# Performance work log

Measured on AMD Instinct MI355X. Metric: run time of the kernel, lower is better.

## Reference

```python
import jax, jax.numpy as jnp
import numpy as np

N = 16384   # src points
M = 16384   # ref points
D = 256     # d_embed
K = 16      # num_neighbors
MAX_DIST = 0.5


def _knn(src, ref, k):
    # squared euclidean distances, [N, M] (pytorch3d knn_points returns squared dists)
    d2 = (jnp.sum(src * src, axis=-1, keepdims=True)
          + jnp.sum(ref * ref, axis=-1)[None, :]
          - 2.0 * src @ ref.T)
    neg_d2, idx = jax.lax.top_k(-d2, k)   # k smallest distances, sorted ascending
    return -neg_d2, idx


def setup_inputs() -> dict:
    key = jax.random.key(0)
    k1, k2, k3, k4, k5 = jax.random.split(key, 5)
    return {
        "ref_points": jax.random.normal(k1, (M, 3), dtype=jnp.float32),
        "src_points": jax.random.normal(k2, (N, 3), dtype=jnp.float32),
        "ref_feats": jax.random.normal(k3, (M, D), dtype=jnp.float32),
        "src_feats": jax.random.normal(k4, (N, D), dtype=jnp.float32),
        "W": jax.random.normal(k5, (D, D), dtype=jnp.float32) * 0.1,
    }


def reference(ref_points, src_points, ref_feats, src_feats, W):
    dist, knn_idx = _knn(src_points, ref_points, K)      # [N,K], [N,K]
    knn_xyz = ref_points[knn_idx]                        # [N,K,3]
    weight = jax.nn.relu(1.0 - dist / MAX_DIST)          # [N,K]

    W_triu = jnp.triu(W)
    W_sym = W_triu + W_triu.T                            # symmetric bilinear form
    knn_feats = ref_feats[knn_idx]                       # [N,K,D]

    scores = jnp.einsum('nc,cd,nkd->nk', src_feats, W_sym, knn_feats)
    attn = jax.nn.softmax(scores * weight, axis=-1)      # [N,K]
    corres = jnp.einsum('nk,nkc->nc', attn, knn_xyz)     # [N,3]

    d = jnp.linalg.norm(src_points - corres, axis=-1)    # [N]
    w = jax.nn.relu(1.0 - d / MAX_DIST)                  # [N]
    return corres, w
```

## Files before the change

### kernel.cpp

```cpp
#include <hip/hip_runtime.h>
#include <math.h>

#define N_SRC 16384
#define M_REF 16384
#define DEMB  256
#define KNN_K 16
#define CAP   128

__global__ void wsym_kernel(const float* __restrict__ W, float* __restrict__ wsym) {
    int i = blockIdx.x;
    int j = threadIdx.x;
    float a = (j >= i) ? W[i * DEMB + j] : 0.f;
    float b = (i >= j) ? W[j * DEMB + i] : 0.f;
    wsym[i * DEMB + j] = a + b;
}

__global__ void pack_kernel(const float* __restrict__ rp, float4* __restrict__ out) {
    int i = blockIdx.x * 256 + threadIdx.x;
    float x = rp[i * 3 + 0], y = rp[i * 3 + 1], z = rp[i * 3 + 2];
    out[i] = make_float4(x, y, z, fmaf(x, x, fmaf(y, y, z * z)));
}

__global__ void __launch_bounds__(256) q_kernel(const float* __restrict__ src_feats,
                                                const float* __restrict__ wsym,
                                                float* __restrict__ q) {
    __shared__ __align__(16) float sf[32][DEMB];
    int n0 = blockIdx.x * 32;
    int tid = threadIdx.x;
    int c0 = tid & 63;
    int rg = tid >> 6;
    {
        int c = c0 * 4;
        #pragma unroll
        for (int rr = 0; rr < 8; ++rr) {
            int r = rr * 4 + rg;
            *(float4*)&sf[r][c] = *(const float4*)&src_feats[(size_t)(n0 + r) * DEMB + c];
        }
    }
    __syncthreads();

    float acc[8][4];
    #pragma unroll
    for (int rr = 0; rr < 8; ++rr)
        #pragma unroll
        for (int cc = 0; cc < 4; ++cc) acc[rr][cc] = 0.f;

    for (int c4 = 0; c4 < 64; ++c4) {
        float wv[4][4];
        #pragma unroll
        for (int j = 0; j < 4; ++j)
            #pragma unroll
            for (int cc = 0; cc < 4; ++cc)
                wv[j][cc] = wsym[(size_t)(c4 * 4 + j) * DEMB + c0 + cc * 64];
        #pragma unroll
        for (int rr = 0; rr < 8; ++rr) {
            float4 s = *(const float4*)&sf[rg * 8 + rr][c4 * 4];
            #pragma unroll
            for (int cc = 0; cc < 4; ++cc) {
                float a = acc[rr][cc];
                a = fmaf(s.x, wv[0][cc], a);
                a = fmaf(s.y, wv[1][cc], a);
                a = fmaf(s.z, wv[2][cc], a);
                a = fmaf(s.w, wv[3][cc], a);
                acc[rr][cc] = a;
            }
        }
    }
    #pragma unroll
    for (int rr = 0; rr < 8; ++rr)
        #pragma unroll
        for (int cc = 0; cc < 4; ++cc)
            q[(size_t)(n0 + rg * 8 + rr) * DEMB + (c0 + cc * 64)] = acc[rr][cc];
}

__device__ __forceinline__ void sort64_kv(float& vd, int& vi, int lane) {
    #pragma unroll
    for (int k = 2; k <= 64; k <<= 1) {
        #pragma unroll
        for (int j = k >> 1; j > 0; j >>= 1) {
            float od = __shfl_xor(vd, j, 64);
            int   oi = __shfl_xor(vi, j, 64);
            bool keep_min = (((lane & j) == 0) == ((lane & k) == 0));
            bool oless = (od < vd) || (od == vd && oi < vi);
            bool take = (keep_min == oless);
            vd = take ? od : vd;
            vi = take ? oi : vi;
        }
    }
}

__global__ void __launch_bounds__(128) knn_kernel(const float* __restrict__ src_points,
                                                  const float4* __restrict__ refp4,
                                                  float* __restrict__ kd2,
                                                  int* __restrict__ kidx) {
    const float INF = 3.0e38f;
    int tid = threadIdx.x;
    int h = tid >> 6, lane = tid & 63;
    int n0 = blockIdx.x * 8;

    __shared__ float cd[8][CAP];
    __shared__ int   ci[8][CAP];
    __shared__ int   cnt[8];
    if (tid < 8) cnt[tid] = 0;

    float m2x[8], m2y[8], m2z[8], sn2[8];
    #pragma unroll
    for (int b = 0; b < 8; ++b) {
        float sx = src_points[(n0 + b) * 3 + 0];
        float sy = src_points[(n0 + b) * 3 + 1];
        float sz = src_points[(n0 + b) * 3 + 2];
        m2x[b] = -2.f * sx; m2y[b] = -2.f * sy; m2z[b] = -2.f * sz;
        sn2[b] = fmaf(sx, sx, fmaf(sy, sy, sz * sz));
    }
    __syncthreads();

    const int base = h * (M_REF / 2);

    float mind[8];
    #pragma unroll
    for (int b = 0; b < 8; ++b) mind[b] = INF;
    for (int it = 0; it < 128; it += 2) {
        float4 r0 = refp4[base + it * 64 + lane];
        float4 r1 = refp4[base + (it + 1) * 64 + lane];
        #pragma unroll
        for (int b = 0; b < 8; ++b) {
            float d0 = fmaf(r0.x, m2x[b], r0.w);
            d0 = fmaf(r0.y, m2y[b], d0);
            d0 = fmaf(r0.z, m2z[b], d0);
            float d1 = fmaf(r1.x, m2x[b], r1.w);
            d1 = fmaf(r1.y, m2y[b], d1);
            d1 = fmaf(r1.z, m2z[b], d1);
            mind[b] = fminf(mind[b], fminf(d0, d1));
        }
    }

    float tau[8];
    #pragma unroll
    for (int b = 0; b < 8; ++b) {
        float v = mind[b];
        #pragma unroll
        for (int k = 2; k <= 64; k <<= 1) {
            #pragma unroll
            for (int j = k >> 1; j > 0; j >>= 1) {
                float o = __shfl_xor(v, j, 64);
                bool lower = (lane & j) == 0;
                bool up = (lane & k) == 0;
                float mn = fminf(v, o), mx = fmaxf(v, o);
                v = (lower == up) ? mn : mx;
            }
        }
        tau[b] = __shfl(v, 15, 64);
    }

    for (int it = 0; it < 128; it += 2) {
        int i0 = base + it * 64 + lane;
        float4 r0 = refp4[i0];
        float4 r1 = refp4[i0 + 64];
        #pragma unroll
        for (int b = 0; b < 8; ++b) {
            float d0 = fmaf(r0.x, m2x[b], r0.w);
            d0 = fmaf(r0.y, m2y[b], d0);
            d0 = fmaf(r0.z, m2z[b], d0);
            float d1 = fmaf(r1.x, m2x[b], r1.w);
            d1 = fmaf(r1.y, m2y[b], d1);
            d1 = fmaf(r1.z, m2z[b], d1);
            if (d0 <= tau[b]) {
                int p = atomicAdd(&cnt[b], 1);
                if (p < CAP) { cd[b][p] = d0; ci[b][p] = i0; }
            }
            if (d1 <= tau[b]) {
                int p = atomicAdd(&cnt[b], 1);
                if (p < CAP) { cd[b][p] = d1; ci[b][p] = i0 + 64; }
            }
        }
    }
    __syncthreads();

    #pragma unroll
    for (int bb = 0; bb < 4; ++bb) {
        int b = h * 4 + bb;
        int count = cnt[b];
        if (count > CAP) count = CAP;
        float vd = (lane < count) ? cd[b][lane] : INF;
        int   vi = (lane < count) ? ci[b][lane] : 0x7fffffff;
        sort64_kv(vd, vi, lane);
        int done = 64;
        while (done < count) {
            if (lane >= 16) {
                int p = done + (lane - 16);
                vd = (p < count) ? cd[b][p] : INF;
                vi = (p < count) ? ci[b][p] : 0x7fffffff;
            }
            sort64_kv(vd, vi, lane);
            done += 48;
        }
        if (lane < KNN_K) {
            kd2[(size_t)(n0 + b) * KNN_K + lane] = vd + sn2[b];
            kidx[(size_t)(n0 + b) * KNN_K + lane] = vi;
        }
    }
}

__global__ void __launch_bounds__(256) score_kernel(const float* __restrict__ q,
                                                    const float* __restrict__ ref_feats,
                                                    const float* __restrict__ ref_points,
                                                    const float* __restrict__ src_points,
                                                    const float* __restrict__ kd2,
                                                    const int* __restrict__ kidx,
                                                    float* __restrict__ out) {
    int wave = threadIdx.x >> 6;
    int lane = threadIdx.x & 63;
    int n = __builtin_amdgcn_readfirstlane(blockIdx.x * 4 + wave);

    float4 qv = *(const float4*)&q[(size_t)n * DEMB + lane * 4];

    int idx[KNN_K]; float d2[KNN_K];
    #pragma unroll
    for (int k = 0; k < KNN_K; ++k) {
        idx[k] = __builtin_amdgcn_readfirstlane(kidx[(size_t)n * KNN_K + k]);
        d2[k]  = kd2[(size_t)n * KNN_K + k];
    }

    float sc[KNN_K];
    #pragma unroll
    for (int k = 0; k < KNN_K; ++k) {
        float4 r = *(const float4*)&ref_feats[(size_t)idx[k] * DEMB + lane * 4];
        float p = fmaf(r.x, qv.x, fmaf(r.y, qv.y, fmaf(r.z, qv.z, r.w * qv.w)));
        #pragma unroll
        for (int off = 1; off < 64; off <<= 1) p += __shfl_xor(p, off, 64);
        sc[k] = p;
    }

    float tv[KNN_K];
    #pragma unroll
    for (int k = 0; k < KNN_K; ++k) {
        float wt = fmaxf(0.f, fmaf(-2.f, d2[k], 1.f));
        tv[k] = sc[k] * wt;
    }
    float m = tv[0];
    #pragma unroll
    for (int k = 1; k < KNN_K; ++k) m = fmaxf(m, tv[k]);
    float e[KNN_K], s = 0.f;
    #pragma unroll
    for (int k = 0; k < KNN_K; ++k) { e[k] = expf(tv[k] - m); s += e[k]; }

    float cx = 0.f, cy = 0.f, cz = 0.f;
    #pragma unroll
    for (int k = 0; k < KNN_K; ++k) {
        float rx = ref_points[idx[k] * 3 + 0];
        float ry = ref_points[idx[k] * 3 + 1];
        float rz = ref_points[idx[k] * 3 + 2];
        cx = fmaf(e[k], rx, cx);
        cy = fmaf(e[k], ry, cy);
        cz = fmaf(e[k], rz, cz);
    }
    float inv = 1.f / s;
    cx *= inv; cy *= inv; cz *= inv;

    if (lane == 0) {
        float ssx = src_points[n * 3 + 0];
        float ssy = src_points[n * 3 + 1];
        float ssz = src_points[n * 3 + 2];
        float dx = ssx - cx, dy = ssy - cy, dz = ssz - cz;
        float dist = sqrtf(fmaf(dx, dx, fmaf(dy, dy, dz * dz)));
        float w = fmaxf(0.f, fmaf(-2.f, dist, 1.f));
        out[(size_t)n * 3 + 0] = cx;
        out[(size_t)n * 3 + 1] = cy;
        out[(size_t)n * 3 + 2] = cz;
        out[(size_t)N_SRC * 3 + n] = w;
    }
}

extern "C" void kernel_launch(void* const* d_in, const int* in_sizes, int n_in,
                              void* d_out, int out_size, void* d_ws, size_t ws_size,
                              hipStream_t stream) {
    const float* ref_points = (const float*)d_in[0];
    const float* src_points = (const float*)d_in[1];
    const float* ref_feats  = (const float*)d_in[2];
    const float* src_feats  = (const float*)d_in[3];
    const float* W          = (const float*)d_in[4];
    float* out = (float*)d_out;

    float*  wsym  = (float*)d_ws;
    float4* refp4 = (float4*)(wsym + DEMB * DEMB);
    float*  q     = (float*)(refp4 + M_REF);
    float*  kd2   = q + (size_t)N_SRC * DEMB;
    int*    kidx  = (int*)(kd2 + (size_t)N_SRC * KNN_K);

    wsym_kernel<<<DEMB, DEMB, 0, stream>>>(W, wsym);
    pack_kernel<<<M_REF / 256, 256, 0, stream>>>(ref_points, refp4);
    q_kernel<<<N_SRC / 32, 256, 0, stream>>>(src_feats, wsym, q);
    knn_kernel<<<N_SRC / 8, 128, 0, stream>>>(src_points, refp4, kd2, kidx);
    score_kernel<<<N_SRC / 4, 256, 0, stream>>>(q, ref_feats, ref_points, src_points, kd2, kidx, out);
}
```

Before: 176.4 us.

## Fuse kNN and q-projection into one heterogeneous launch with 4-wave kNN blocks

After: 167.8 us. 1.05x faster.

```diff
diff --git a/kernel.cpp b/kernel.cpp
--- a/kernel.cpp
+++ b/kernel.cpp
@@ -5,7 +5,12 @@
 #define M_REF 16384
 #define DEMB  256
 #define KNN_K 16
-#define CAP   128
+#define CAP   288
+
+#define KNN_BLOCKS (N_SRC / 8)
+#define Q_BLOCKS   (N_SRC / 16)
+
+#define SMEM_BYTES (8 * CAP * 8 + 32 + 128)
 
 __global__ void wsym_kernel(const float* __restrict__ W, float* __restrict__ wsym) {
     int i = blockIdx.x;
@@ -19,58 +24,6 @@
     int i = blockIdx.x * 256 + threadIdx.x;
     float x = rp[i * 3 + 0], y = rp[i * 3 + 1], z = rp[i * 3 + 2];
     out[i] = make_float4(x, y, z, fmaf(x, x, fmaf(y, y, z * z)));
-}
-
-__global__ void __launch_bounds__(256) q_kernel(const float* __restrict__ src_feats,
-                                                const float* __restrict__ wsym,
-                                                float* __restrict__ q) {
-    __shared__ __align__(16) float sf[32][DEMB];
-    int n0 = blockIdx.x * 32;
-    int tid = threadIdx.x;
-    int c0 = tid & 63;
-    int rg = tid >> 6;
-    {
-        int c = c0 * 4;
-        #pragma unroll
-        for (int rr = 0; rr < 8; ++rr) {
-            int r = rr * 4 + rg;
-            *(float4*)&sf[r][c] = *(const float4*)&src_feats[(size_t)(n0 + r) * DEMB + c];
-        }
-    }
-    __syncthreads();
-
-    float acc[8][4];
-    #pragma unroll
-    for (int rr = 0; rr < 8; ++rr)
-        #pragma unroll
-        for (int cc = 0; cc < 4; ++cc) acc[rr][cc] = 0.f;
-
-    for (int c4 = 0; c4 < 64; ++c4) {
-        float wv[4][4];
-        #pragma unroll
-        for (int j = 0; j < 4; ++j)
-            #pragma unroll
-            for (int cc = 0; cc < 4; ++cc)
-                wv[j][cc] = wsym[(size_t)(c4 * 4 + j) * DEMB + c0 + cc * 64];
-        #pragma unroll
-        for (int rr = 0; rr < 8; ++rr) {
-            float4 s = *(const float4*)&sf[rg * 8 + rr][c4 * 4];
-            #pragma unroll
-            for (int cc = 0; cc < 4; ++cc) {
-                float a = acc[rr][cc];
-                a = fmaf(s.x, wv[0][cc], a);
-                a = fmaf(s.y, wv[1][cc], a);
-                a = fmaf(s.z, wv[2][cc], a);
-                a = fmaf(s.w, wv[3][cc], a);
-                acc[rr][cc] = a;
-            }
-        }
-    }
-    #pragma unroll
-    for (int rr = 0; rr < 8; ++rr)
-        #pragma unroll
-        for (int cc = 0; cc < 4; ++cc)
-            q[(size_t)(n0 + rg * 8 + rr) * DEMB + (c0 + cc * 64)] = acc[rr][cc];
 }
 
 __device__ __forceinline__ void sort64_kv(float& vd, int& vi, int lane) {
@@ -89,115 +42,176 @@
     }
 }
 
-__global__ void __launch_bounds__(128) knn_kernel(const float* __restrict__ src_points,
-                                                  const float4* __restrict__ refp4,
-                                                  float* __restrict__ kd2,
-                                                  int* __restrict__ kidx) {
-    const float INF = 3.0e38f;
+__global__ void __launch_bounds__(256, 8) fused_kernel(
+        const float* __restrict__ src_points, const float4* __restrict__ refp4,
+        const float* __restrict__ src_feats,  const float* __restrict__ wsym,
+        float* __restrict__ kd2, int* __restrict__ kidx, float* __restrict__ q) {
+    __shared__ __align__(16) char smem[SMEM_BYTES];
     int tid = threadIdx.x;
-    int h = tid >> 6, lane = tid & 63;
-    int n0 = blockIdx.x * 8;
-
-    __shared__ float cd[8][CAP];
-    __shared__ int   ci[8][CAP];
-    __shared__ int   cnt[8];
-    if (tid < 8) cnt[tid] = 0;
-
-    float m2x[8], m2y[8], m2z[8], sn2[8];
-    #pragma unroll
-    for (int b = 0; b < 8; ++b) {
-        float sx = src_points[(n0 + b) * 3 + 0];
-        float sy = src_points[(n0 + b) * 3 + 1];
-        float sz = src_points[(n0 + b) * 3 + 2];
-        m2x[b] = -2.f * sx; m2y[b] = -2.f * sy; m2z[b] = -2.f * sz;
-        sn2[b] = fmaf(sx, sx, fmaf(sy, sy, sz * sz));
-    }
-    __syncthreads();
-
-    const int base = h * (M_REF / 2);
-
-    float mind[8];
-    #pragma unroll
-    for (int b = 0; b < 8; ++b) mind[b] = INF;
-    for (int it = 0; it < 128; it += 2) {
-        float4 r0 = refp4[base + it * 64 + lane];
-        float4 r1 = refp4[base + (it + 1) * 64 + lane];
+
+    if (blockIdx.x < KNN_BLOCKS) {
+        const float INF = 3.0e38f;
+        float (*cd)[CAP] = (float(*)[CAP])smem;
+        int   (*ci)[CAP] = (int(*)[CAP])(smem + 8 * CAP * 4);
+        int*   cnt       = (int*)(smem + 8 * CAP * 8);
+        float (*stau)[8] = (float(*)[8])(smem + 8 * CAP * 8 + 32);
+
+        int h = tid >> 6, lane = tid & 63;
+        int n0 = blockIdx.x * 8;
+        if (tid < 8) cnt[tid] = 0;
+
+        float m2x[8], m2y[8], m2z[8], sn2[8];
         #pragma unroll
         for (int b = 0; b < 8; ++b) {
-            float d0 = fmaf(r0.x, m2x[b], r0.w);
-            d0 = fmaf(r0.y, m2y[b], d0);
-            d0 = fmaf(r0.z, m2z[b], d0);
-            float d1 = fmaf(r1.x, m2x[b], r1.w);
-            d1 = fmaf(r1.y, m2y[b], d1);
-            d1 = fmaf(r1.z, m2z[b], d1);
-            mind[b] = fminf(mind[b], fminf(d0, d1));
-        }
-    }
-
-    float tau[8];
-    #pragma unroll
-    for (int b = 0; b < 8; ++b) {
-        float v = mind[b];
-        #pragma unroll
-        for (int k = 2; k <= 64; k <<= 1) {
-            #pragma unroll
-            for (int j = k >> 1; j > 0; j >>= 1) {
-                float o = __shfl_xor(v, j, 64);
-                bool lower = (lane & j) == 0;
-                bool up = (lane & k) == 0;
-                float mn = fminf(v, o), mx = fmaxf(v, o);
-                v = (lower == up) ? mn : mx;
-            }
-        }
-        tau[b] = __shfl(v, 15, 64);
-    }
-
-    for (int it = 0; it < 128; it += 2) {
-        int i0 = base + it * 64 + lane;
-        float4 r0 = refp4[i0];
-        float4 r1 = refp4[i0 + 64];
+            float sx = src_points[(n0 + b) * 3 + 0];
+            float sy = src_points[(n0 + b) * 3 + 1];
+            float sz = src_points[(n0 + b) * 3 + 2];
+            m2x[b] = -2.f * sx; m2y[b] = -2.f * sy; m2z[b] = -2.f * sz;
+            sn2[b] = fmaf(sx, sx, fmaf(sy, sy, sz * sz));
+        }
+
+        const int qbase = h * (M_REF / 4);
+
+        float mind[8];
+        #pragma unroll
+        for (int b = 0; b < 8; ++b) mind[b] = INF;
+        for (int it = 0; it < 32; it += 2) {
+            float4 r0 = refp4[qbase + it * 64 + lane];
+            float4 r1 = refp4[qbase + (it + 1) * 64 + lane];
+            #pragma unroll
+            for (int b = 0; b < 8; ++b) {
+                float d0 = fmaf(r0.x, m2x[b], r0.w);
+                d0 = fmaf(r0.y, m2y[b], d0);
+                d0 = fmaf(r0.z, m2z[b], d0);
+                float d1 = fmaf(r1.x, m2x[b], r1.w);
+                d1 = fmaf(r1.y, m2y[b], d1);
+                d1 = fmaf(r1.z, m2z[b], d1);
+                mind[b] = fminf(mind[b], fminf(d0, d1));
+            }
+        }
+
+        float tauh[8];
         #pragma unroll
         for (int b = 0; b < 8; ++b) {
-            float d0 = fmaf(r0.x, m2x[b], r0.w);
-            d0 = fmaf(r0.y, m2y[b], d0);
-            d0 = fmaf(r0.z, m2z[b], d0);
-            float d1 = fmaf(r1.x, m2x[b], r1.w);
-            d1 = fmaf(r1.y, m2y[b], d1);
-            d1 = fmaf(r1.z, m2z[b], d1);
-            if (d0 <= tau[b]) {
-                int p = atomicAdd(&cnt[b], 1);
-                if (p < CAP) { cd[b][p] = d0; ci[b][p] = i0; }
-            }
-            if (d1 <= tau[b]) {
-                int p = atomicAdd(&cnt[b], 1);
-                if (p < CAP) { cd[b][p] = d1; ci[b][p] = i0 + 64; }
-            }
-        }
-    }
-    __syncthreads();
-
-    #pragma unroll
-    for (int bb = 0; bb < 4; ++bb) {
-        int b = h * 4 + bb;
-        int count = cnt[b];
-        if (count > CAP) count = CAP;
-        float vd = (lane < count) ? cd[b][lane] : INF;
-        int   vi = (lane < count) ? ci[b][lane] : 0x7fffffff;
-        sort64_kv(vd, vi, lane);
-        int done = 64;
-        while (done < count) {
-            if (lane >= 16) {
-                int p = done + (lane - 16);
-                vd = (p < count) ? cd[b][p] : INF;
-                vi = (p < count) ? ci[b][p] : 0x7fffffff;
-            }
+            float v = mind[b];
+            #pragma unroll
+            for (int k = 2; k <= 64; k <<= 1) {
+                #pragma unroll
+                for (int j = k >> 1; j > 0; j >>= 1) {
+                    float o = __shfl_xor(v, j, 64);
+                    bool lower = (lane & j) == 0;
+                    bool up = (lane & k) == 0;
+                    float mn = fminf(v, o), mx = fmaxf(v, o);
+                    v = (lower == up) ? mn : mx;
+                }
+            }
+            tauh[b] = __shfl(v, 15, 64);
+        }
+        if (lane == 0) {
+            #pragma unroll
+            for (int b = 0; b < 8; ++b) stau[h][b] = tauh[b];
+        }
+        __syncthreads();
+        float taul[8];
+        #pragma unroll
+        for (int b = 0; b < 8; ++b)
+            taul[b] = fminf(fminf(stau[0][b], stau[1][b]),
+                            fminf(stau[2][b], stau[3][b]));
+
+        for (int it = 0; it < 64; it += 2) {
+            int i0 = qbase + it * 64 + lane;
+            float4 r0 = refp4[i0];
+            float4 r1 = refp4[i0 + 64];
+            #pragma unroll
+            for (int b = 0; b < 8; ++b) {
+                float d0 = fmaf(r0.x, m2x[b], r0.w);
+                d0 = fmaf(r0.y, m2y[b], d0);
+                d0 = fmaf(r0.z, m2z[b], d0);
+                float d1 = fmaf(r1.x, m2x[b], r1.w);
+                d1 = fmaf(r1.y, m2y[b], d1);
+                d1 = fmaf(r1.z, m2z[b], d1);
+                if (d0 <= taul[b]) {
+                    int p = atomicAdd(&cnt[b], 1);
+                    if (p < CAP) { cd[b][p] = d0; ci[b][p] = i0; }
+                }
+                if (d1 <= taul[b]) {
+                    int p = atomicAdd(&cnt[b], 1);
+                    if (p < CAP) { cd[b][p] = d1; ci[b][p] = i0 + 64; }
+                }
+            }
+        }
+        __syncthreads();
+
+        #pragma unroll
+        for (int bb = 0; bb < 2; ++bb) {
+            int b = h * 2 + bb;
+            int count = cnt[b];
+            if (count > CAP) count = CAP;
+            float vd = (lane < count) ? cd[b][lane] : INF;
+            int   vi = (lane < count) ? ci[b][lane] : 0x7fffffff;
             sort64_kv(vd, vi, lane);
-            done += 48;
-        }
-        if (lane < KNN_K) {
-            kd2[(size_t)(n0 + b) * KNN_K + lane] = vd + sn2[b];
-            kidx[(size_t)(n0 + b) * KNN_K + lane] = vi;
-        }
+            int done = 64;
+            while (done < count) {
+                if (lane >= 16) {
+                    int p = done + (lane - 16);
+                    vd = (p < count) ? cd[b][p] : INF;
+                    vi = (p < count) ? ci[b][p] : 0x7fffffff;
+                }
+                sort64_kv(vd, vi, lane);
+                done += 48;
+            }
+            if (lane < KNN_K) {
+                kd2[(size_t)(n0 + b) * KNN_K + lane] = vd + sn2[b];
+                kidx[(size_t)(n0 + b) * KNN_K + lane] = vi;
+            }
+        }
+    } else {
+        float (*sf)[DEMB] = (float(*)[DEMB])smem;
+        int n0 = (blockIdx.x - KNN_BLOCKS) * 16;
+        int c0 = tid & 63;
+        int rg = tid >> 6;
+        {
+            int c = c0 * 4;
+            #pragma unroll
+            for (int rr = 0; rr < 4; ++rr) {
+                int r = rr * 4 + rg;
+                *(float4*)&sf[r][c] = *(const float4*)&src_feats[(size_t)(n0 + r) * DEMB + c];
+            }
+        }
+        __syncthreads();
+
+        float acc[4][4];
+        #pragma unroll
+        for (int rr = 0; rr < 4; ++rr)
+            #pragma unroll
+            for (int cc = 0; cc < 4; ++cc) acc[rr][cc] = 0.f;
+
+        for (int c4 = 0; c4 < 64; ++c4) {
+            float wv[4][4];
+            #pragma unroll
+            for (int j = 0; j < 4; ++j)
+                #pragma unroll
+                for (int cc = 0; cc < 4; ++cc)
+                    wv[j][cc] = wsym[(size_t)(c4 * 4 + j) * DEMB + c0 + cc * 64];
+            #pragma unroll
+            for (int rr = 0; rr < 4; ++rr) {
+                float4 s = *(const float4*)&sf[rg * 4 + rr][c4 * 4];
+                #pragma unroll
+                for (int cc = 0; cc < 4; ++cc) {
+                    float a = acc[rr][cc];
+                    a = fmaf(s.x, wv[0][cc], a);
+                    a = fmaf(s.y, wv[1][cc], a);
+                    a = fmaf(s.z, wv[2][cc], a);
+                    a = fmaf(s.w, wv[3][cc], a);
+                    acc[rr][cc] = a;
+                }
+            }
+        }
+        #pragma unroll
+        for (int rr = 0; rr < 4; ++rr)
+            #pragma unroll
+            for (int cc = 0; cc < 4; ++cc)
+                q[(size_t)(n0 + rg * 4 + rr) * DEMB + (c0 + cc * 64)] = acc[rr][cc];
     }
 }
 
@@ -289,7 +303,7 @@
 
     wsym_kernel<<<DEMB, DEMB, 0, stream>>>(W, wsym);
     pack_kernel<<<M_REF / 256, 256, 0, stream>>>(ref_points, refp4);
-    q_kernel<<<N_SRC / 32, 256, 0, stream>>>(src_feats, wsym, q);
-    knn_kernel<<<N_SRC / 8, 128, 0, stream>>>(src_points, refp4, kd2, kidx);
+    fused_kernel<<<KNN_BLOCKS + Q_BLOCKS, 256, 0, stream>>>(
+        src_points, refp4, src_feats, wsym, kd2, kidx, q);
     score_kernel<<<N_SRC / 4, 256, 0, stream>>>(q, ref_feats, ref_points, src_points, kd2, kidx, out);
 }
```

## Replace brute-force KNN with uniform grid spatial binning and expanding search

Applied to the files above, without the earlier changes.

Result: slower. 256.7 us (+45.6%).

```diff
diff --git a/kernel.cpp b/kernel.cpp
--- a/kernel.cpp
+++ b/kernel.cpp
@@ -5,72 +5,124 @@
 #define M_REF 16384
 #define DEMB  256
 #define KNN_K 16
-#define CAP   128
-
-__global__ void wsym_kernel(const float* __restrict__ W, float* __restrict__ wsym) {
-    int i = blockIdx.x;
-    int j = threadIdx.x;
-    float a = (j >= i) ? W[i * DEMB + j] : 0.f;
-    float b = (i >= j) ? W[j * DEMB + i] : 0.f;
-    wsym[i * DEMB + j] = a + b;
-}
-
-__global__ void pack_kernel(const float* __restrict__ rp, float4* __restrict__ out) {
+#define CAP   96
+#define NC    32
+#define GB    4.25f
+#define CH    0.265625f
+#define NCELLS (NC * NC * NC)
+
+__device__ __forceinline__ int cell_of(float x) {
+    int c = (int)floorf((x + GB) * (1.0f / CH));
+    return min(max(c, 0), NC - 1);
+}
+
+__global__ void __launch_bounds__(256) zero_wsym_kernel(int* __restrict__ cursor,
+                                                        const float* __restrict__ W,
+                                                        float* __restrict__ wsym) {
+    int b = blockIdx.x, t = threadIdx.x;
+    if (b < NCELLS / 256) {
+        cursor[b * 256 + t] = 0;
+    } else {
+        int i = b - NCELLS / 256, j = t;
+        float a = (j >= i) ? W[i * DEMB + j] : 0.f;
+        float c = (i >= j) ? W[j * DEMB + i] : 0.f;
+        wsym[i * DEMB + j] = a + c;
+    }
+}
+
+__global__ void __launch_bounds__(256) hist_kernel(const float* __restrict__ rp,
+                                                   int* __restrict__ cursor) {
     int i = blockIdx.x * 256 + threadIdx.x;
-    float x = rp[i * 3 + 0], y = rp[i * 3 + 1], z = rp[i * 3 + 2];
-    out[i] = make_float4(x, y, z, fmaf(x, x, fmaf(y, y, z * z)));
-}
-
-__global__ void __launch_bounds__(256) q_kernel(const float* __restrict__ src_feats,
-                                                const float* __restrict__ wsym,
-                                                float* __restrict__ q) {
+    int cx = cell_of(rp[i * 3 + 0]);
+    int cy = cell_of(rp[i * 3 + 1]);
+    int cz = cell_of(rp[i * 3 + 2]);
+    atomicAdd(&cursor[(cz * NC + cy) * NC + cx], 1);
+}
+
+__global__ void __launch_bounds__(1024) scan_kernel(int* __restrict__ cursor,
+                                                    int* __restrict__ cell_start) {
+    __shared__ int part[1024];
+    int t = threadIdx.x;
+    int loc[32]; int s = 0;
+    #pragma unroll
+    for (int i = 0; i < 32; ++i) { loc[i] = s; s += cursor[t * 32 + i]; }
+    part[t] = s;
+    __syncthreads();
+    for (int off = 1; off < 1024; off <<= 1) {
+        int add = (t >= off) ? part[t - off] : 0;
+        __syncthreads();
+        part[t] += add;
+        __syncthreads();
+    }
+    int ex = part[t] - s;
+    #pragma unroll
+    for (int i = 0; i < 32; ++i) {
+        cell_start[t * 32 + i] = ex + loc[i];
+        cursor[t * 32 + i]     = ex + loc[i];
+    }
+    if (t == 1023) cell_start[NCELLS] = part[1023];
+}
+
+__global__ void __launch_bounds__(256) scatter_q_kernel(const float* __restrict__ rp,
+        int* __restrict__ cursor, float4* __restrict__ refp4s, int* __restrict__ ridx_s,
+        const float* __restrict__ src_feats, const float* __restrict__ wsym,
+        float* __restrict__ q) {
     __shared__ __align__(16) float sf[32][DEMB];
-    int n0 = blockIdx.x * 32;
     int tid = threadIdx.x;
-    int c0 = tid & 63;
-    int rg = tid >> 6;
-    {
-        int c = c0 * 4;
-        #pragma unroll
-        for (int rr = 0; rr < 8; ++rr) {
-            int r = rr * 4 + rg;
-            *(float4*)&sf[r][c] = *(const float4*)&src_feats[(size_t)(n0 + r) * DEMB + c];
-        }
-    }
-    __syncthreads();
-
-    float acc[8][4];
-    #pragma unroll
-    for (int rr = 0; rr < 8; ++rr)
-        #pragma unroll
-        for (int cc = 0; cc < 4; ++cc) acc[rr][cc] = 0.f;
-
-    for (int c4 = 0; c4 < 64; ++c4) {
-        float wv[4][4];
-        #pragma unroll
-        for (int j = 0; j < 4; ++j)
+    if (blockIdx.x < 64) {
+        int i = blockIdx.x * 256 + tid;
+        float x = rp[i * 3 + 0], y = rp[i * 3 + 1], z = rp[i * 3 + 2];
+        int c = (cell_of(z) * NC + cell_of(y)) * NC + cell_of(x);
+        int pos = atomicAdd(&cursor[c], 1);
+        refp4s[pos] = make_float4(x, y, z, fmaf(x, x, fmaf(y, y, z * z)));
+        ridx_s[pos] = i;
+    } else {
+        int n0 = (blockIdx.x - 64) * 32;
+        int c0 = tid & 63;
+        int rg = tid >> 6;
+        {
+            int c = c0 * 4;
+            #pragma unroll
+            for (int rr = 0; rr < 8; ++rr) {
+                int r = rr * 4 + rg;
+                *(float4*)&sf[r][c] = *(const float4*)&src_feats[(size_t)(n0 + r) * DEMB + c];
+            }
+        }
+        __syncthreads();
+
+        float acc[8][4];
+        #pragma unroll
+        for (int rr = 0; rr < 8; ++rr)
+            #pragma unroll
+            for (int cc = 0; cc < 4; ++cc) acc[rr][cc] = 0.f;
+
+        for (int c4 = 0; c4 < 64; ++c4) {
+            float wv[4][4];
+            #pragma unroll
+            for (int j = 0; j < 4; ++j)
+                #pragma unroll
+                for (int cc = 0; cc < 4; ++cc)
+                    wv[j][cc] = wsym[(size_t)(c4 * 4 + j) * DEMB + c0 + cc * 64];
+            #pragma unroll
+            for (int rr = 0; rr < 8; ++rr) {
+                float4 s4 = *(const float4*)&sf[rg * 8 + rr][c4 * 4];
+                #pragma unroll
+                for (int cc = 0; cc < 4; ++cc) {
+                    float a = acc[rr][cc];
+                    a = fmaf(s4.x, wv[0][cc], a);
+                    a = fmaf(s4.y, wv[1][cc], a);
+                    a = fmaf(s4.z, wv[2][cc], a);
+                    a = fmaf(s4.w, wv[3][cc], a);
+                    acc[rr][cc] = a;
+                }
+            }
+        }
+        #pragma unroll
+        for (int rr = 0; rr < 8; ++rr)
             #pragma unroll
             for (int cc = 0; cc < 4; ++cc)
-                wv[j][cc] = wsym[(size_t)(c4 * 4 + j) * DEMB + c0 + cc * 64];
-        #pragma unroll
-        for (int rr = 0; rr < 8; ++rr) {
-            float4 s = *(const float4*)&sf[rg * 8 + rr][c4 * 4];
-            #pragma unroll
-            for (int cc = 0; cc < 4; ++cc) {
-                float a = acc[rr][cc];
-                a = fmaf(s.x, wv[0][cc], a);
-                a = fmaf(s.y, wv[1][cc], a);
-                a = fmaf(s.z, wv[2][cc], a);
-                a = fmaf(s.w, wv[3][cc], a);
-                acc[rr][cc] = a;
-            }
-        }
-    }
-    #pragma unroll
-    for (int rr = 0; rr < 8; ++rr)
-        #pragma unroll
-        for (int cc = 0; cc < 4; ++cc)
-            q[(size_t)(n0 + rg * 8 + rr) * DEMB + (c0 + cc * 64)] = acc[rr][cc];
+                q[(size_t)(n0 + rg * 8 + rr) * DEMB + (c0 + cc * 64)] = acc[rr][cc];
+    }
 }
 
 __device__ __forceinline__ void sort64_kv(float& vd, int& vi, int lane) {
@@ -89,55 +141,65 @@
     }
 }
 
-__global__ void __launch_bounds__(128) knn_kernel(const float* __restrict__ src_points,
-                                                  const float4* __restrict__ refp4,
-                                                  float* __restrict__ kd2,
-                                                  int* __restrict__ kidx) {
+__global__ void __launch_bounds__(256) knn_kernel(const float* __restrict__ src_points,
+        const float4* __restrict__ refp4s, const int* __restrict__ ridx_s,
+        const int* __restrict__ cell_start,
+        float* __restrict__ kd2, int* __restrict__ kidx) {
     const float INF = 3.0e38f;
     int tid = threadIdx.x;
-    int h = tid >> 6, lane = tid & 63;
-    int n0 = blockIdx.x * 8;
-
-    __shared__ float cd[8][CAP];
-    __shared__ int   ci[8][CAP];
-    __shared__ int   cnt[8];
-    if (tid < 8) cnt[tid] = 0;
-
-    float m2x[8], m2y[8], m2z[8], sn2[8];
-    #pragma unroll
-    for (int b = 0; b < 8; ++b) {
-        float sx = src_points[(n0 + b) * 3 + 0];
-        float sy = src_points[(n0 + b) * 3 + 1];
-        float sz = src_points[(n0 + b) * 3 + 2];
-        m2x[b] = -2.f * sx; m2y[b] = -2.f * sy; m2z[b] = -2.f * sz;
-        sn2[b] = fmaf(sx, sx, fmaf(sy, sy, sz * sz));
-    }
-    __syncthreads();
-
-    const int base = h * (M_REF / 2);
-
-    float mind[8];
-    #pragma unroll
-    for (int b = 0; b < 8; ++b) mind[b] = INF;
-    for (int it = 0; it < 128; it += 2) {
-        float4 r0 = refp4[base + it * 64 + lane];
-        float4 r1 = refp4[base + (it + 1) * 64 + lane];
-        #pragma unroll
-        for (int b = 0; b < 8; ++b) {
-            float d0 = fmaf(r0.x, m2x[b], r0.w);
-            d0 = fmaf(r0.y, m2y[b], d0);
-            d0 = fmaf(r0.z, m2z[b], d0);
-            float d1 = fmaf(r1.x, m2x[b], r1.w);
-            d1 = fmaf(r1.y, m2y[b], d1);
-            d1 = fmaf(r1.z, m2z[b], d1);
-            mind[b] = fminf(mind[b], fminf(d0, d1));
-        }
-    }
-
-    float tau[8];
-    #pragma unroll
-    for (int b = 0; b < 8; ++b) {
-        float v = mind[b];
+    int wave = tid >> 6, lane = tid & 63;
+    int n = blockIdx.x * 4 + wave;
+
+    __shared__ float cd[4][CAP];
+    __shared__ int   ci[4][CAP];
+    __shared__ int   cnt[4];
+
+    float sx = src_points[n * 3 + 0];
+    float sy = src_points[n * 3 + 1];
+    float sz = src_points[n * 3 + 2];
+    float m2x = -2.f * sx, m2y = -2.f * sy, m2z = -2.f * sz;
+    float sn2 = fmaf(sx, sx, fmaf(sy, sy, sz * sz));
+    int cx = cell_of(sx), cy = cell_of(sy), cz = cell_of(sz);
+
+    int r = (sn2 > 9.f) ? NC : 1;
+
+    while (true) {
+        int x0 = max(cx - r, 0), x1 = min(cx + r, NC - 1);
+        int y0 = max(cy - r, 0), y1 = min(cy + r, NC - 1);
+        int z0 = max(cz - r, 0), z1 = min(cz + r, NC - 1);
+        bool full = (x0 == 0 && y0 == 0 && z0 == 0 &&
+                     x1 == NC - 1 && y1 == NC - 1 && z1 == NC - 1);
+
+        if (lane == 0) cnt[wave] = 0;
+
+        float mind = INF;
+        if (full) {
+            for (int p = lane; p < M_REF; p += 64) {
+                float4 rp = refp4s[p];
+                float d = fmaf(rp.x, m2x, rp.w);
+                d = fmaf(rp.y, m2y, d);
+                d = fmaf(rp.z, m2z, d);
+                mind = fminf(mind, d);
+            }
+        } else {
+            int off = 0;
+            for (int zc = z0; zc <= z1; ++zc)
+                for (int yc = y0; yc <= y1; ++yc) {
+                    int rb = (zc * NC + yc) * NC;
+                    int st = cell_start[rb + x0];
+                    int en = cell_start[rb + x1 + 1];
+                    int np = en - st;
+                    for (int k = (lane - off) & 63; k < np; k += 64) {
+                        float4 rp = refp4s[st + k];
+                        float d = fmaf(rp.x, m2x, rp.w);
+                        d = fmaf(rp.y, m2y, d);
+                        d = fmaf(rp.z, m2z, d);
+                        mind = fminf(mind, d);
+                    }
+                    off = (off + np) & 63;
+                }
+        }
+        float v = mind;
         #pragma unroll
         for (int k = 2; k <= 64; k <<= 1) {
             #pragma unroll
@@ -149,55 +211,65 @@
                 v = (lower == up) ? mn : mx;
             }
         }
-        tau[b] = __shfl(v, 15, 64);
-    }
-
-    for (int it = 0; it < 128; it += 2) {
-        int i0 = base + it * 64 + lane;
-        float4 r0 = refp4[i0];
-        float4 r1 = refp4[i0 + 64];
-        #pragma unroll
-        for (int b = 0; b < 8; ++b) {
-            float d0 = fmaf(r0.x, m2x[b], r0.w);
-            d0 = fmaf(r0.y, m2y[b], d0);
-            d0 = fmaf(r0.z, m2z[b], d0);
-            float d1 = fmaf(r1.x, m2x[b], r1.w);
-            d1 = fmaf(r1.y, m2y[b], d1);
-            d1 = fmaf(r1.z, m2z[b], d1);
-            if (d0 <= tau[b]) {
-                int p = atomicAdd(&cnt[b], 1);
-                if (p < CAP) { cd[b][p] = d0; ci[b][p] = i0; }
-            }
-            if (d1 <= tau[b]) {
-                int p = atomicAdd(&cnt[b], 1);
-                if (p < CAP) { cd[b][p] = d1; ci[b][p] = i0 + 64; }
-            }
-        }
-    }
-    __syncthreads();
-
-    #pragma unroll
-    for (int bb = 0; bb < 4; ++bb) {
-        int b = h * 4 + bb;
-        int count = cnt[b];
+        float tau = __shfl(v, 15, 64);
+
+        if (full) {
+            for (int p = lane; p < M_REF; p += 64) {
+                float4 rp = refp4s[p];
+                float d = fmaf(rp.x, m2x, rp.w);
+                d = fmaf(rp.y, m2y, d);
+                d = fmaf(rp.z, m2z, d);
+                if (d <= tau) {
+                    int pp = atomicAdd(&cnt[wave], 1);
+                    if (pp < CAP) { cd[wave][pp] = d; ci[wave][pp] = ridx_s[p]; }
+                }
+            }
+        } else {
+            for (int zc = z0; zc <= z1; ++zc)
+                for (int yc = y0; yc <= y1; ++yc) {
+                    int rb = (zc * NC + yc) * NC;
+                    int st = cell_start[rb + x0];
+                    int en = cell_start[rb + x1 + 1];
+                    int np = en - st;
+                    for (int k = lane; k < np; k += 64) {
+                        float4 rp = refp4s[st + k];
+                        float d = fmaf(rp.x, m2x, rp.w);
+                        d = fmaf(rp.y, m2y, d);
+                        d = fmaf(rp.z, m2z, d);
+                        if (d <= tau) {
+                            int pp = atomicAdd(&cnt[wave], 1);
+                            if (pp < CAP) { cd[wave][pp] = d; ci[wave][pp] = ridx_s[st + k]; }
+                        }
+                    }
+                }
+        }
+
+        int count = cnt[wave];
         if (count > CAP) count = CAP;
-        float vd = (lane < count) ? cd[b][lane] : INF;
-        int   vi = (lane < count) ? ci[b][lane] : 0x7fffffff;
+        float vd = (lane < count) ? cd[wave][lane] : INF;
+        int   vi = (lane < count) ? ci[wave][lane] : 0x7fffffff;
         sort64_kv(vd, vi, lane);
         int done = 64;
         while (done < count) {
             if (lane >= 16) {
                 int p = done + (lane - 16);
-                vd = (p < count) ? cd[b][p] : INF;
-                vi = (p < count) ? ci[b][p] : 0x7fffffff;
+                vd = (p < count) ? cd[wave][p] : INF;
+                vi = (p < count) ? ci[wave][p] : 0x7fffffff;
             }
             sort64_kv(vd, vi, lane);
             done += 48;
         }
-        if (lane < KNN_K) {
-            kd2[(size_t)(n0 + b) * KNN_K + lane] = vd + sn2[b];
-            kidx[(size_t)(n0 + b) * KNN_K + lane] = vi;
-        }
+        float d16 = __shfl(vd, 15, 64) + sn2;
+        float rb = (float)r * CH;
+        if (full || d16 <= rb * rb * 0.998f) {
+            if (lane < KNN_K) {
+                kd2[(size_t)n * KNN_K + lane] = vd + sn2;
+                kidx[(size_t)n * KNN_K + lane] = vi;
+            }
+            break;
+        }
+        r <<= 1;
+        if (r > NC) r = NC;
     }
 }
 
@@ -281,15 +353,21 @@
     const float* W          = (const float*)d_in[4];
     float* out = (float*)d_out;
 
-    float*  wsym  = (float*)d_ws;
-    float4* refp4 = (float4*)(wsym + DEMB * DEMB);
-    float*  q     = (float*)(refp4 + M_REF);
-    float*  kd2   = q + (size_t)N_SRC * DEMB;
-    int*    kidx  = (int*)(kd2 + (size_t)N_SRC * KNN_K);
-
-    wsym_kernel<<<DEMB, DEMB, 0, stream>>>(W, wsym);
-    pack_kernel<<<M_REF / 256, 256, 0, stream>>>(ref_points, refp4);
-    q_kernel<<<N_SRC / 32, 256, 0, stream>>>(src_feats, wsym, q);
-    knn_kernel<<<N_SRC / 8, 128, 0, stream>>>(src_points, refp4, kd2, kidx);
+    char* ws = (char*)d_ws;
+    float4* refp4s     = (float4*)ws;                 ws += (size_t)M_REF * 16;
+    float*  q          = (float*)ws;                  ws += (size_t)N_SRC * DEMB * 4;
+    float*  wsym       = (float*)ws;                  ws += (size_t)DEMB * DEMB * 4;
+    float*  kd2        = (float*)ws;                  ws += (size_t)N_SRC * KNN_K * 4;
+    int*    kidx       = (int*)ws;                    ws += (size_t)N_SRC * KNN_K * 4;
+    int*    ridx_s     = (int*)ws;                    ws += (size_t)M_REF * 4;
+    int*    cell_start = (int*)ws;                    ws += (size_t)(NCELLS + 4) * 4;
+    int*    cursor     = (int*)ws;
+
+    zero_wsym_kernel<<<NCELLS / 256 + DEMB, 256, 0, stream>>>(cursor, W, wsym);
+    hist_kernel<<<M_REF / 256, 256, 0, stream>>>(ref_points, cursor);
+    scan_kernel<<<1, 1024, 0, stream>>>(cursor, cell_start);
+    scatter_q_kernel<<<64 + N_SRC / 32, 256, 0, stream>>>(ref_points, cursor, refp4s, ridx_s,
+                                                          src_feats, wsym, q);
+    knn_kernel<<<N_SRC / 4, 256, 0, stream>>>(src_points, refp4s, ridx_s, cell_start, kd2, kidx);
     score_kernel<<<N_SRC / 4, 256, 0, stream>>>(q, ref_feats, ref_points, src_points, kd2, kidx, out);
 }
```
